# Kernel optimization log

Hardware: AMD Instinct MI355X
Metric: run time of the kernel (lower is better)

The kernel has to match this reference:

```python
import jax, jax.numpy as jnp
import numpy as np

B, S, D = 32, 512, 1024
H = 1024
Hh = H // 2
CYC = 3
EPS = 1e-6


def setup_inputs() -> dict:
    key = jax.random.key(0)
    ks = jax.random.split(key, 16)
    def rn(k, shape, scale):
        return (jax.random.normal(k, shape, dtype=jnp.float32) * scale)
    inp = {
        'x': rn(ks[0], (B, S, D), 1.0),
        'W_x': rn(ks[1], (D, H), 1.0 / np.sqrt(D)),
        'b_x': jnp.zeros((H,), jnp.float32),
        'W_h': rn(ks[2], (H, H), 1.0 / np.sqrt(H)),
        'b_h': jnp.zeros((H,), jnp.float32),
        'W_r': rn(ks[3], (D + H, H), 1.0 / np.sqrt(D + H)),
        'b_r': jnp.zeros((H,), jnp.float32),
        'W_s': rn(ks[4], (H, 3), 1.0 / np.sqrt(H)),
        'b_s': jnp.zeros((3,), jnp.float32),
        # Mobius coefficients (cycles, [re,im], Hh): a,d near identity, b,c small
        'mob_a': rn(ks[5], (CYC, 2, Hh), 0.01).at[:, 0, :].add(1.0),
        'mob_b': rn(ks[6], (CYC, 2, Hh), 0.01),
        'mob_c': rn(ks[7], (CYC, 2, Hh), 0.01),
        'mob_d': rn(ks[8], (CYC, 2, Hh), 0.01).at[:, 0, :].add(1.0),
        'W_o': rn(ks[9], (H, H), 1.0 / np.sqrt(H)),
        'b_o': jnp.zeros((H,), jnp.float32),
    }
    return inp


def _mobius(zo, zp, a, b, c, d):
    # elementwise complex Mobius transform z -> (a z + b) / (c z + d)
    a_re, a_im = a[0], a[1]
    b_re, b_im = b[0], b[1]
    c_re, c_im = c[0], c[1]
    d_re, d_im = d[0], d[1]
    num_re = a_re * zo - a_im * zp + b_re
    num_im = a_re * zp + a_im * zo + b_im
    den_re = c_re * zo - c_im * zp + d_re
    den_im = c_re * zp + c_im * zo + d_im
    den2 = den_re * den_re + den_im * den_im + EPS
    return ((num_re * den_re + num_im * den_im) / den2,
            (num_im * den_re - num_re * den_im) / den2)


def reference(x, W_x, b_x, W_h, b_h, W_r, b_r, W_s, b_s,
              mob_a, mob_b, mob_c, mob_d, W_o, b_o):
    Bx = x.shape[0]
    scales = jnp.array([1.0, 0.5, 0.25], dtype=x.dtype)

    def step(h, x_t):
        omega_h, pi_h = h                                  # (B, Hh) each
        h_cat = jnp.concatenate([omega_h, pi_h], axis=-1)  # (B, H)
        x_proj = jnp.tanh(x_t @ W_x + b_x)
        cand = jnp.tanh(x_proj + h_cat @ W_h + b_h)
        zo, zp = cand[:, :Hh], cand[:, Hh:]
        for k in range(CYC):
            zo, zp = _mobius(zo, zp, mob_a[k], mob_b[k], mob_c[k], mob_d[k])
        # adaptive evolution rate
        r = jax.nn.sigmoid(jnp.concatenate([x_t, h_cat], axis=-1) @ W_r + b_r)
        # multiscale evolution: softmax-mixed decay scale per batch element
        w = jax.nn.softmax(h_cat @ W_s + b_s, axis=-1)     # (B, 3)
        rate = r * (w @ scales)[:, None]                   # (B, H)
        ro, rp = rate[:, :Hh], rate[:, Hh:]
        new_o = (1.0 - ro) * omega_h + ro * zo
        new_p = (1.0 - rp) * pi_h + rp * zp
        out = jnp.tanh(jnp.concatenate([new_o, new_p], axis=-1) @ W_o + b_o)
        return (new_o, new_p), out

    h0 = (jnp.zeros((Bx, Hh), x.dtype), jnp.zeros((Bx, Hh), x.dtype))
    (of, pf), ys = jax.lax.scan(step, h0, jnp.swapaxes(x, 0, 1))
    output = jnp.swapaxes(ys, 0, 1)                        # (B, S, H)
    return output, of, pf
```

## Files before the change

### kernel.cpp

```cpp
#include <hip/hip_runtime.h>
#include <math.h>

typedef unsigned short u16;
typedef unsigned int u32;
typedef __attribute__((ext_vector_type(8))) short bf16x8;
typedef __attribute__((ext_vector_type(4))) float f32x4;

#define B_N 32
#define S_N 512
#define H_N 1024
#define HH_N 512
#define FRAME (B_N*H_N)
#define GBLK 32
#define EPS_F 1e-6f

#define MFMA16(a,b,c) __builtin_amdgcn_mfma_f32_16x16x32_bf16((a),(b),(c),0,0,0)
#define ATOM_ST(p,v) __hip_atomic_store((p),(v),__ATOMIC_RELAXED,__HIP_MEMORY_SCOPE_AGENT)

static __device__ __forceinline__ u16 f2bu(float v){
  union{float f; unsigned u;} x; x.f = v;
  unsigned r = x.u + 0x7FFFu + ((x.u>>16)&1u);
  return (u16)(r>>16);
}
static __device__ __forceinline__ float bu2f(u16 s){
  union{unsigned u; float f;} x; x.u = ((unsigned)s)<<16; return x.f;
}
static __device__ __forceinline__ bf16x8 ld8(const u16* p){
  return *reinterpret_cast<const bf16x8*>(p);
}
static __device__ __forceinline__ void cvt8(const float* p, bf16x8& hi, bf16x8& lo){
  #pragma unroll
  for(int j=0;j<8;j++){
    float v = p[j];
    u16 h = f2bu(v);
    hi[j] = (short)h;
    lo[j] = (short)f2bu(v - bu2f(h));
  }
}

__global__ __launch_bounds__(256) void k_trcvt(const float* __restrict__ src,
    u16* __restrict__ dh, u16* __restrict__ dl){
  __shared__ float tile[32][33];
  int c0 = blockIdx.x*32, k0 = blockIdx.y*32;
  int tx = threadIdx.x & 31, ty = threadIdx.x >> 5;
  for(int i=ty;i<32;i+=8) tile[i][tx] = src[(size_t)(k0+i)*H_N + c0 + tx];
  __syncthreads();
  for(int i=ty;i<32;i+=8){
    float v = tile[tx][i];
    u16 h = f2bu(v);
    dh[(size_t)(c0+i)*H_N + k0 + tx] = h;
    if(dl) dl[(size_t)(c0+i)*H_N + k0 + tx] = f2bu(v - bu2f(h));
  }
}

__global__ __launch_bounds__(256) void k_wspack(const float* __restrict__ Ws,
                                                u16* __restrict__ wsp){
  int gid = blockIdx.x*256 + threadIdx.x;
  int j = gid & 7, l = (gid>>3) & 63, ks = gid >> 9;
  int lr = l & 15, lg = l >> 4;
  int k = ks*32 + lg*8 + j;
  wsp[gid] = (lr < 3) ? f2bu(Ws[k*3 + lr]) : (u16)0;
}

__global__ __launch_bounds__(256) void k_pre(const float* __restrict__ x,
    const u16* __restrict__ WxTh, const u16* __restrict__ WxTl,
    const u16* __restrict__ WrxTh, const u16* __restrict__ WrxTl,
    const float* __restrict__ b_x,
    u16* __restrict__ xp, u16* __restrict__ xplo,
    u16* __restrict__ xr, u16* __restrict__ xrlo){
  int tid = threadIdx.x, l = tid&63, wid = tid>>6;
  int wm = wid>>1, wn = wid&1, lr = l&15, lg = l>>4;
  int mbase = blockIdx.y*64 + wm*32;
  int nblk = blockIdx.x*64;
  bool isX = (nblk < H_N);
  int nbase = nblk + wn*32;
  const u16* WTh = isX? WxTh : WrxTh;
  const u16* WTl = isX? WxTl : WrxTl;
  int nw0 = isX? nbase : (nbase - H_N);
  const float* ar[2]; const u16* brh[2]; const u16* brl[2];
  #pragma unroll
  for(int mt=0;mt<2;mt++){
    int m = mbase + mt*16 + lr;
    ar[mt] = x + ((size_t)(m & (B_N-1))*S_N + (m>>5))*H_N;
  }
  #pragma unroll
  for(int nt=0;nt<2;nt++){
    brh[nt] = WTh + (size_t)(nw0 + nt*16 + lr)*H_N;
    brl[nt] = WTl + (size_t)(nw0 + nt*16 + lr)*H_N;
  }
  f32x4 zz = {0.f,0.f,0.f,0.f};
  f32x4 acc[2][2] = {{zz,zz},{zz,zz}};
  for(int ks=0;ks<32;ks++){
    int ke = ks*32 + lg*8;
    bf16x8 ah[2], al[2], bh[2], bl[2];
    #pragma unroll
    for(int mt=0;mt<2;mt++) cvt8(ar[mt]+ke, ah[mt], al[mt]);
    #pragma unroll
    for(int nt=0;nt<2;nt++){ bh[nt] = ld8(brh[nt]+ke); bl[nt] = ld8(brl[nt]+ke); }
    #pragma unroll
    for(int mt=0;mt<2;mt++)
      #pragma unroll
      for(int nt=0;nt<2;nt++){
        acc[mt][nt] = MFMA16(ah[mt],bh[nt],acc[mt][nt]);
        acc[mt][nt] = MFMA16(al[mt],bh[nt],acc[mt][nt]);
        acc[mt][nt] = MFMA16(ah[mt],bl[nt],acc[mt][nt]);
      }
  }
  #pragma unroll
  for(int mt=0;mt<2;mt++)
    #pragma unroll
    for(int nt=0;nt<2;nt++){
      int n = nbase + nt*16 + lr;
      #pragma unroll
      for(int i=0;i<4;i++){
        int m = mbase + mt*16 + lg*4 + i;
        size_t idx = (size_t)m*H_N + (isX? n : (n - H_N));
        float v = acc[mt][nt][i];
        if(isX){
          float tv = tanhf(v + b_x[n]);
          u16 h = f2bu(tv);
          xp[idx] = h;
          if(xplo) xplo[idx] = f2bu(tv - bu2f(h));
        }else{
          u16 h = f2bu(v);
          xr[idx] = h;
          if(xrlo) xrlo[idx] = f2bu(v - bu2f(h));
        }
      }
    }
}

__global__ __launch_bounds__(256) void k_fin(const u16* __restrict__ hall,
    const u16* __restrict__ WoTh, const u16* __restrict__ WoTl,
    const float* __restrict__ b_o, float* __restrict__ out){
  int tid = threadIdx.x, l = tid&63, wid = tid>>6;
  int wm = wid>>1, wn = wid&1, lr = l&15, lg = l>>4;
  int mbase = blockIdx.y*64 + wm*32;
  int nbase = blockIdx.x*64 + wn*32;
  size_t arowB[2]; const u16* brh[2]; const u16* brl[2];
  #pragma unroll
  for(int mt=0;mt<2;mt++){
    int m = mbase + mt*16 + lr;
    arowB[mt] = (size_t)(m>>5)*FRAME + (size_t)(m&31)*32;
  }
  #pragma unroll
  for(int nt=0;nt<2;nt++){
    brh[nt] = WoTh + (size_t)(nbase + nt*16 + lr)*H_N;
    brl[nt] = WoTl + (size_t)(nbase + nt*16 + lr)*H_N;
  }
  int lgadd = (lg>>1)*1024 + (lg&1)*8;
  f32x4 zz = {0.f,0.f,0.f,0.f};
  f32x4 acc[2][2] = {{zz,zz},{zz,zz}};
  for(int ks=0;ks<32;ks++){
    int ke = ks*32 + lg*8;
    int abase = (2*(ks&15))*1024 + lgadd + ((ks>=16)?16:0);
    #pragma unroll
    for(int mt=0;mt<2;mt++){
      bf16x8 a = ld8(hall + arowB[mt] + abase);
      #pragma unroll
      for(int nt=0;nt<2;nt++){
        acc[mt][nt] = MFMA16(a, ld8(brh[nt]+ke), acc[mt][nt]);
        acc[mt][nt] = MFMA16(a, ld8(brl[nt]+ke), acc[mt][nt]);
      }
    }
  }
  #pragma unroll
  for(int mt=0;mt<2;mt++)
    #pragma unroll
    for(int nt=0;nt<2;nt++){
      int n = nbase + nt*16 + lr;
      float bo = b_o[n];
      #pragma unroll
      for(int i=0;i<4;i++){
        int m = mbase + mt*16 + lg*4 + i;
        int b = m & (B_N-1), t = m >> 5;
        out[((size_t)b*S_N + t)*H_N + n] = tanhf(acc[mt][nt][i] + bo);
      }
    }
}

__global__ __launch_bounds__(256) void k_recur(
    const u16* __restrict__ xp, const u16* __restrict__ xplo0,
    const u16* __restrict__ xr, const u16* __restrict__ xrlo0, int xlostep,
    const u16* __restrict__ WhTh, const u16* __restrict__ WhTl,
    const u16* __restrict__ WrTh, const u16* __restrict__ wsp,
    const float* __restrict__ b_h, const float* __restrict__ b_r,
    const float* __restrict__ b_s,
    const float* __restrict__ mob_a, const float* __restrict__ mob_b,
    const float* __restrict__ mob_c, const float* __restrict__ mob_d,
    const u16* __restrict__ zhi, u16* __restrict__ lob,
    u16* __restrict__ hall, float* __restrict__ hf, int* __restrict__ arr)
{
  __shared__ float Cred[32*84];
  __shared__ float Cs[32*84];
  __shared__ float mobp[16*25];
  __shared__ float bias[64];
  __shared__ float sbar[32];
  __shared__ float bsv[3];
  __shared__ float hfL[32][33];
  int tid = threadIdx.x, bid = blockIdx.x;
  int P0 = bid*16;
  int l = tid&63, kq = tid>>6;
  int lr = l&15, lg = l>>4;

  for(int idx=tid; idx<384; idx+=256){
    int j = idx/24, c = idx%24, cyc = c>>3, q = c&7;
    const float* arrp = (q<2)? mob_a : (q<4)? mob_b : (q<6)? mob_c : mob_d;
    mobp[j*25 + c] = arrp[cyc*H_N + (q&1)*HH_N + P0 + j];
  }
  if(tid < 64){
    int grp = tid>>4, jj = tid&15;
    bias[tid] = ((grp<2)? b_h : b_r)[P0 + jj + ((grp&1)? HH_N : 0)];
  } else if(tid < 67){
    bsv[tid-64] = b_s[tid-64];
  }
  for(int idx=tid; idx<32*33; idx+=256) (&hfL[0][0])[idx] = 0.f;

  const u16* bhOh = WhTh + (size_t)(P0 + lr)*H_N;
  const u16* bhOl = WhTl + (size_t)(P0 + lr)*H_N;
  const u16* bhPh = WhTh + (size_t)(P0 + HH_N + lr)*H_N;
  const u16* bhPl = WhTl + (size_t)(P0 + HH_N + lr)*H_N;
  const u16* brO  = WrTh + (size_t)(P0 + lr)*H_N;
  const u16* brP  = WrTh + (size_t)(P0 + HH_N + lr)*H_N;
  const u16* wps  = wsp + (size_t)(kq*8)*512 + l*8;
  int lgadd = (lg>>1)*1024 + (lg&1)*8 + ((kq>=2)?16:0);
  int row0t = lr*32, row1t = (16+lr)*32;
  int erow = tid>>3, ejj = (tid&7)*2;
  size_t ei0 = (size_t)erow*H_N + P0 + ejj;
  size_t ei1 = ei0 + HH_N;

  __syncthreads();

  for(int t=0; t<S_N; t++){
    const u16* hihB = (t==0)? zhi : (hall + (size_t)(t-1)*FRAME);
    const u16* hilB = lob + (size_t)(t&1)*FRAME;
    const u16* xp_t   = xp + (size_t)t*FRAME;
    const u16* xr_t   = xr + (size_t)t*FRAME;
    const u16* xplo_t = xplo0 + (size_t)t*xlostep;
    const u16* xrlo_t = xrlo0 + (size_t)t*xlostep;

    u32 pxpL = *(const u32*)(xp_t   + ei0);
    u32 pxpH = *(const u32*)(xp_t   + ei1);
    u32 ploL = *(const u32*)(xplo_t + ei0);
    u32 ploH = *(const u32*)(xplo_t + ei1);
    u32 pxrL = *(const u32*)(xr_t   + ei0);
    u32 pxrH = *(const u32*)(xr_t   + ei1);
    u32 prlL = *(const u32*)(xrlo_t + ei0);
    u32 prlH = *(const u32*)(xrlo_t + ei1);

    f32x4 zz = {0.f,0.f,0.f,0.f};
    f32x4 cO0=zz,cO1=zz,cP0=zz,cP1=zz,rOa=zz,rOb=zz,rPa=zz,rPb=zz,sA=zz,sB=zz;
    #pragma unroll
    for(int i=0;i<8;i++){
      int ke = (kq*8+i)*32 + lg*8;
      int abase = (2*((kq&1)*8+i))*1024 + lgadd;
      bf16x8 ah0 = ld8(hihB + abase + row0t);
      bf16x8 ah1 = ld8(hihB + abase + row1t);
      bf16x8 al0 = ld8(hilB + abase + row0t);
      bf16x8 al1 = ld8(hilB + abase + row1t);
      bf16x8 fOh = ld8(bhOh+ke), fOl = ld8(bhOl+ke);
      bf16x8 fPh = ld8(bhPh+ke), fPl = ld8(bhPl+ke);
      bf16x8 frO_ = ld8(brO+ke), frP_ = ld8(brP+ke);
      bf16x8 fs   = ld8(wps + i*512);
      cO0 = MFMA16(ah0,fOh,cO0); cO0 = MFMA16(al0,fOh,cO0); cO0 = MFMA16(ah0,fOl,cO0);
      cO1 = MFMA16(ah1,fOh,cO1); cO1 = MFMA16(al1,fOh,cO1); cO1 = MFMA16(ah1,fOl,cO1);
      cP0 = MFMA16(ah0,fPh,cP0); cP0 = MFMA16(al0,fPh,cP0); cP0 = MFMA16(ah0,fPl,cP0);
      cP1 = MFMA16(ah1,fPh,cP1); cP1 = MFMA16(al1,fPh,cP1); cP1 = MFMA16(ah1,fPl,cP1);
      rOa = MFMA16(ah0,frO_,rOa); rOa = MFMA16(al0,frO_,rOa);
      rOb = MFMA16(ah1,frO_,rOb); rOb = MFMA16(al1,frO_,rOb);
      rPa = MFMA16(ah0,frP_,rPa); rPa = MFMA16(al0,frP_,rPa);
      rPb = MFMA16(ah1,frP_,rPb); rPb = MFMA16(al1,frP_,rPb);
      sA  = MFMA16(ah0,fs, sA);  sA  = MFMA16(al0,fs, sA);
      sB  = MFMA16(ah1,fs, sB);  sB  = MFMA16(al1,fs, sB);
    }

    __syncthreads();
    float* D = (kq&1)? Cs : Cred;
    if(kq < 2){
      #pragma unroll
      for(int i=0;i<4;i++){
        int r0 = (lg*4+i)*84, r1 = (16+lg*4+i)*84;
        D[r0 +      lr] = cO0[i];  D[r1 +      lr] = cO1[i];
        D[r0 + 16 + lr] = cP0[i];  D[r1 + 16 + lr] = cP1[i];
        D[r0 + 32 + lr] = rOa[i];  D[r1 + 32 + lr] = rOb[i];
        D[r0 + 48 + lr] = rPa[i];  D[r1 + 48 + lr] = rPb[i];
        D[r0 + 64 + lr] = sA[i];   D[r1 + 64 + lr] = sB[i];
      }
    }
    __syncthreads();
    if(kq >= 2){
      #pragma unroll
      for(int i=0;i<4;i++){
        int r0 = (lg*4+i)*84, r1 = (16+lg*4+i)*84;
        D[r0 +      lr] += cO0[i];  D[r1 +      lr] += cO1[i];
        D[r0 + 16 + lr] += cP0[i];  D[r1 + 16 + lr] += cP1[i];
        D[r0 + 32 + lr] += rOa[i];  D[r1 + 32 + lr] += rOb[i];
        D[r0 + 48 + lr] += rPa[i];  D[r1 + 48 + lr] += rPb[i];
        D[r0 + 64 + lr] += sA[i];   D[r1 + 64 + lr] += sB[i];
      }
    }
    __syncthreads();
    for(int idx=tid; idx<2560; idx+=256){
      int r = idx/80, c = idx - r*80;
      Cred[r*84+c] += Cs[r*84+c];
    }
    __syncthreads();

    if(tid < 32){
      float l0 = Cred[tid*84+64] + bsv[0];
      float l1 = Cred[tid*84+65] + bsv[1];
      float l2 = Cred[tid*84+66] + bsv[2];
      float mx = fmaxf(l0, fmaxf(l1,l2));
      float e0 = expf(l0-mx), e1 = expf(l1-mx), e2 = expf(l2-mx);
      sbar[tid] = (e0 + 0.5f*e1 + 0.25f*e2) / (e0+e1+e2);
    }
    __syncthreads();

    {
      float sb = sbar[erow];
      u16 nob[2], npb[2], loO[2], loP[2];
      #pragma unroll
      for(int d=0; d<2; d++){
        int j = ejj + d;
        float xpv0 = bu2f((u16)(pxpL>>(16*d))) + bu2f((u16)(ploL>>(16*d)));
        float xpv1 = bu2f((u16)(pxpH>>(16*d))) + bu2f((u16)(ploH>>(16*d)));
        float xrv0 = bu2f((u16)(pxrL>>(16*d))) + bu2f((u16)(prlL>>(16*d)));
        float xrv1 = bu2f((u16)(pxrH>>(16*d))) + bu2f((u16)(prlH>>(16*d)));
        float zo = tanhf(xpv0 + Cred[erow*84 + j]      + bias[j]);
        float zp = tanhf(xpv1 + Cred[erow*84 + 16 + j] + bias[16+j]);
        float ro = 1.f/(1.f + expf(-(xrv0 + Cred[erow*84 + 32 + j] + bias[32+j])));
        float rp = 1.f/(1.f + expf(-(xrv1 + Cred[erow*84 + 48 + j] + bias[48+j])));
        const float* mp = &mobp[j*25];
        #pragma unroll
        for(int cy=0;cy<3;cy++){
          float are=mp[cy*8+0], aim=mp[cy*8+1], bre=mp[cy*8+2], bim=mp[cy*8+3];
          float cre=mp[cy*8+4], cim=mp[cy*8+5], dre=mp[cy*8+6], dim_=mp[cy*8+7];
          float nre = are*zo - aim*zp + bre;
          float nim = are*zp + aim*zo + bim;
          float de  = cre*zo - cim*zp + dre;
          float di  = cre*zp + cim*zo + dim_;
          float inv = 1.f/(de*de + di*di + EPS_F);
          float nzo = (nre*de + nim*di)*inv;
          float nzp = (nim*de - nre*di)*inv;
          zo = nzo; zp = nzp;
        }
        ro *= sb; rp *= sb;
        float ho = hfL[erow][j], hp2 = hfL[erow][16+j];
        float no  = (1.f-ro)*ho + ro*zo;
        float np2 = (1.f-rp)*hp2 + rp*zp;
        hfL[erow][j] = no; hfL[erow][16+j] = np2;
        nob[d] = f2bu(no);  npb[d] = f2bu(np2);
        loO[d] = f2bu(no  - bu2f(nob[d]));
        loP[d] = f2bu(np2 - bu2f(npb[d]));
      }
      size_t bb = (size_t)bid*1024 + (size_t)erow*32 + ejj;
      u16* hallT = hall + (size_t)t*FRAME;
      u16* lonT  = lob + (size_t)((t+1)&1)*FRAME;
      ATOM_ST((u32*)(hallT + bb),      (u32)nob[0] | ((u32)nob[1]<<16));
      ATOM_ST((u32*)(hallT + bb + 16), (u32)npb[0] | ((u32)npb[1]<<16));
      ATOM_ST((u32*)(lonT  + bb),      (u32)loO[0] | ((u32)loO[1]<<16));
      ATOM_ST((u32*)(lonT  + bb + 16), (u32)loP[0] | ((u32)loP[1]<<16));
    }

    __syncthreads();
    if(tid == 0)
      __hip_atomic_store(&arr[bid<<5], t+1, __ATOMIC_RELEASE, __HIP_MEMORY_SCOPE_AGENT);
    if(tid < GBLK){
      while(__hip_atomic_load(&arr[tid<<5], __ATOMIC_ACQUIRE, __HIP_MEMORY_SCOPE_AGENT) <= t)
        __builtin_amdgcn_s_sleep(1);
    }
    __syncthreads();
  }

  for(int idx=tid; idx<1024; idx+=256){
    int r = idx>>5, c = idx&31;
    int g = (c<16)? (P0+c) : (P0 + HH_N + (c-16));
    hf[(size_t)r*H_N + g] = hfL[r][c];
  }
}

__global__ __launch_bounds__(256) void k_tail(const float* __restrict__ hf,
                                              float* __restrict__ out){
  int i = blockIdx.x*256 + threadIdx.x;
  int b = i >> 10, c = i & 1023;
  float v = hf[(size_t)b*H_N + c];
  size_t base = (size_t)B_N*S_N*H_N;
  size_t idx = (c < HH_N) ? base + (size_t)b*HH_N + c
                          : base + (size_t)B_N*HH_N + (size_t)b*HH_N + (c - HH_N);
  out[idx] = v;
}

extern "C" void kernel_launch(void* const* d_in, const int* in_sizes, int n_in,
                              void* d_out, int out_size, void* d_ws, size_t ws_size,
                              hipStream_t stream)
{
  const float* x    = (const float*)d_in[0];
  const float* W_x  = (const float*)d_in[1];
  const float* b_x  = (const float*)d_in[2];
  const float* W_h  = (const float*)d_in[3];
  const float* b_h  = (const float*)d_in[4];
  const float* W_r  = (const float*)d_in[5];
  const float* b_r  = (const float*)d_in[6];
  const float* W_s  = (const float*)d_in[7];
  const float* b_s  = (const float*)d_in[8];
  const float* mob_a= (const float*)d_in[9];
  const float* mob_b= (const float*)d_in[10];
  const float* mob_c= (const float*)d_in[11];
  const float* mob_d= (const float*)d_in[12];
  const float* W_o  = (const float*)d_in[13];
  const float* b_o  = (const float*)d_in[14];
  float* out = (float*)d_out;

  char* ws = (char*)d_ws;
  size_t off = 0;
  auto carve = [&](size_t bytes)->char*{
    char* p = ws + off; off = (off + bytes + 255) & ~(size_t)255; return p;
  };
  int*   arr  = (int*)carve(4096);
  float* hf   = (float*)carve((size_t)FRAME*sizeof(float));
  u16*   zhi  = (u16*)carve((size_t)FRAME*sizeof(u16));
  u16*   lob  = (u16*)carve((size_t)2*FRAME*sizeof(u16));
  size_t hdr_bytes = off;
  u16*   WhTh = (u16*)carve((size_t)H_N*H_N*sizeof(u16));
  u16*   WhTl = (u16*)carve((size_t)H_N*H_N*sizeof(u16));
  u16*   WrTh = (u16*)carve((size_t)H_N*H_N*sizeof(u16));
  u16*   wsp  = (u16*)carve((size_t)32*512*sizeof(u16));
  u16*   hall = (u16*)carve((size_t)S_N*FRAME*sizeof(u16));
  u16*   xp   = (u16*)carve((size_t)S_N*FRAME*sizeof(u16));
  u16*   xr   = (u16*)carve((size_t)S_N*FRAME*sizeof(u16));
  size_t base_off = off;
  size_t lo_bytes = (size_t)S_N*FRAME*sizeof(u16);
  bool haslo = (ws_size >= base_off + 2*lo_bytes + 4096);
  u16* xplo = nullptr; u16* xrlo = nullptr;
  if(haslo){
    xplo = (u16*)carve(lo_bytes);
    xrlo = (u16*)carve(lo_bytes);
  }

  const size_t WSZ = (size_t)H_N*H_N;
  u16* WxTh  = hall;
  u16* WxTl  = hall + WSZ;
  u16* WrxTh = hall + 2*WSZ;
  u16* WrxTl = hall + 3*WSZ;
  u16* WoTh  = xp;
  u16* WoTl  = xp + WSZ;

  (void)hipMemsetAsync(d_ws, 0, hdr_bytes, stream);

  k_trcvt<<<dim3(32,32),256,0,stream>>>(W_h, WhTh, WhTl);
  k_trcvt<<<dim3(32,32),256,0,stream>>>(W_r + (size_t)H_N*H_N, WrTh, (u16*)nullptr);
  k_trcvt<<<dim3(32,32),256,0,stream>>>(W_x, WxTh, WxTl);
  k_trcvt<<<dim3(32,32),256,0,stream>>>(W_r, WrxTh, WrxTl);
  k_wspack<<<64,256,0,stream>>>(W_s, wsp);
  k_pre<<<dim3(32,256),256,0,stream>>>(x, WxTh, WxTl, WrxTh, WrxTl, b_x,
                                       xp, xplo, xr, xrlo);

  k_recur<<<GBLK,256,0,stream>>>(
      xp, haslo ? xplo : zhi, xr, haslo ? xrlo : zhi, haslo ? FRAME : 0,
      WhTh, WhTl, WrTh, wsp, b_h, b_r, b_s,
      mob_a, mob_b, mob_c, mob_d, zhi, lob, hall, hf, arr);

  k_trcvt<<<dim3(32,32),256,0,stream>>>(W_o, WoTh, WoTl);
  k_fin<<<dim3(16,256),256,0,stream>>>(hall, WoTh, WoTl, b_o, out);
  k_tail<<<128,256,0,stream>>>(hf, out);
}
```

Measured before the change: 5.687 ms.

## Replace grid barrier with per-producer flag polling and fuse partial-sum reduction

Removes the full grid-wide spin barrier at the end of each timestep. Instead, each wave polls the arrival flags of only the producer blocks whose hidden-state chunks it needs and runs the MFMA k-slices as soon as those chunks are ready. The four wave partial sums are now written to separate shared buffers and reduced in a single pass, and every thread computes the softmax scale itself, which removes several __syncthreads. The trade-offs are more polling traffic and data-dependent control flow inside the MFMA loop, and the memory ordering between the relaxed stores and the release flag becomes more delicate.

```diff
diff --git a/kernel.cpp b/kernel.cpp
--- a/kernel.cpp
+++ b/kernel.cpp
@@ -191,11 +191,9 @@
     const u16* __restrict__ zhi, u16* __restrict__ lob,
     u16* __restrict__ hall, float* __restrict__ hf, int* __restrict__ arr)
 {
-  __shared__ float Cred[32*84];
-  __shared__ float Cs[32*84];
+  __shared__ float Cpart[4][2688];
   __shared__ float mobp[16*25];
   __shared__ float bias[64];
-  __shared__ float sbar[32];
   __shared__ float bsv[3];
   __shared__ float hfL[32][33];
   int tid = threadIdx.x, bid = blockIdx.x;
@@ -225,6 +223,7 @@
   const u16* wps  = wsp + (size_t)(kq*8)*512 + l*8;
   int lgadd = (lg>>1)*1024 + (lg&1)*8 + ((kq>=2)?16:0);
   int row0t = lr*32, row1t = (16+lr)*32;
+  int ob = (kq&1)*16;
   int erow = tid>>3, ejj = (tid&7)*2;
   size_t ei0 = (size_t)erow*H_N + P0 + ejj;
   size_t ei1 = ei0 + HH_N;
@@ -250,74 +249,73 @@
 
     f32x4 zz = {0.f,0.f,0.f,0.f};
     f32x4 cO0=zz,cO1=zz,cP0=zz,cP1=zz,rOa=zz,rOb=zz,rPa=zz,rPb=zz,sA=zz,sB=zz;
-    #pragma unroll
-    for(int i=0;i<8;i++){
-      int ke = (kq*8+i)*32 + lg*8;
-      int abase = (2*((kq&1)*8+i))*1024 + lgadd;
-      bf16x8 ah0 = ld8(hihB + abase + row0t);
-      bf16x8 ah1 = ld8(hihB + abase + row1t);
-      bf16x8 al0 = ld8(hilB + abase + row0t);
-      bf16x8 al1 = ld8(hilB + abase + row1t);
-      bf16x8 fOh = ld8(bhOh+ke), fOl = ld8(bhOl+ke);
-      bf16x8 fPh = ld8(bhPh+ke), fPl = ld8(bhPl+ke);
-      bf16x8 frO_ = ld8(brO+ke), frP_ = ld8(brP+ke);
-      bf16x8 fs   = ld8(wps + i*512);
-      cO0 = MFMA16(ah0,fOh,cO0); cO0 = MFMA16(al0,fOh,cO0); cO0 = MFMA16(ah0,fOl,cO0);
-      cO1 = MFMA16(ah1,fOh,cO1); cO1 = MFMA16(al1,fOh,cO1); cO1 = MFMA16(ah1,fOl,cO1);
-      cP0 = MFMA16(ah0,fPh,cP0); cP0 = MFMA16(al0,fPh,cP0); cP0 = MFMA16(ah0,fPl,cP0);
-      cP1 = MFMA16(ah1,fPh,cP1); cP1 = MFMA16(al1,fPh,cP1); cP1 = MFMA16(ah1,fPl,cP1);
-      rOa = MFMA16(ah0,frO_,rOa); rOa = MFMA16(al0,frO_,rOa);
-      rOb = MFMA16(ah1,frO_,rOb); rOb = MFMA16(al1,frO_,rOb);
-      rPa = MFMA16(ah0,frP_,rPa); rPa = MFMA16(al0,frP_,rPa);
-      rPb = MFMA16(ah1,frP_,rPb); rPb = MFMA16(al1,frP_,rPb);
-      sA  = MFMA16(ah0,fs, sA);  sA  = MFMA16(al0,fs, sA);
-      sB  = MFMA16(ah1,fs, sB);  sB  = MFMA16(al1,fs, sB);
-    }
-
+
+    unsigned rem = 0xFFu;
+    while(rem){
+      int f = 0x7fffffff;
+      if(l < 16)
+        f = __hip_atomic_load(&arr[(ob + l)<<5], __ATOMIC_ACQUIRE, __HIP_MEMORY_SCOPE_AGENT);
+      unsigned long long bal = __ballot(f >= t);
+      unsigned own = (unsigned)bal & 0xFFFFu;
+      unsigned pr  = own & (own>>1) & 0x5555u;
+      while(pr){
+        int b2 = __ffs(pr)-1; pr &= pr-1;
+        int i = b2 >> 1;
+        if(!(rem & (1u<<i))) continue;
+        rem &= ~(1u<<i);
+        int ke = (kq*8+i)*32 + lg*8;
+        int abase = (2*((kq&1)*8+i))*1024 + lgadd;
+        bf16x8 ah0 = ld8(hihB + abase + row0t);
+        bf16x8 ah1 = ld8(hihB + abase + row1t);
+        bf16x8 al0 = ld8(hilB + abase + row0t);
+        bf16x8 al1 = ld8(hilB + abase + row1t);
+        bf16x8 fOh = ld8(bhOh+ke), fOl = ld8(bhOl+ke);
+        bf16x8 fPh = ld8(bhPh+ke), fPl = ld8(bhPl+ke);
+        bf16x8 frO_ = ld8(brO+ke), frP_ = ld8(brP+ke);
+        bf16x8 fs   = ld8(wps + i*512);
+        cO0 = MFMA16(ah0,fOh,cO0); cO0 = MFMA16(al0,fOh,cO0); cO0 = MFMA16(ah0,fOl,cO0);
+        cO1 = MFMA16(ah1,fOh,cO1); cO1 = MFMA16(al1,fOh,cO1); cO1 = MFMA16(ah1,fOl,cO1);
+        cP0 = MFMA16(ah0,fPh,cP0); cP0 = MFMA16(al0,fPh,cP0); cP0 = MFMA16(ah0,fPl,cP0);
+        cP1 = MFMA16(ah1,fPh,cP1); cP1 = MFMA16(al1,fPh,cP1); cP1 = MFMA16(ah1,fPl,cP1);
+        rOa = MFMA16(ah0,frO_,rOa); rOa = MFMA16(al0,frO_,rOa);
+        rOb = MFMA16(ah1,frO_,rOb); rOb = MFMA16(al1,frO_,rOb);
+        rPa = MFMA16(ah0,frP_,rPa); rPa = MFMA16(al0,frP_,rPa);
+        rPb = MFMA16(ah1,frP_,rPb); rPb = MFMA16(al1,frP_,rPb);
+        sA  = MFMA16(ah0,fs, sA);  sA  = MFMA16(al0,fs, sA);
+        sB  = MFMA16(ah1,fs, sB);  sB  = MFMA16(al1,fs, sB);
+      }
+      if(rem) __builtin_amdgcn_s_sleep(1);
+    }
+
+    float* W = Cpart[kq];
+    #pragma unroll
+    for(int i=0;i<4;i++){
+      int r0 = (lg*4+i)*84, r1 = (16+lg*4+i)*84;
+      W[r0 +      lr] = cO0[i];  W[r1 +      lr] = cO1[i];
+      W[r0 + 16 + lr] = cP0[i];  W[r1 + 16 + lr] = cP1[i];
+      W[r0 + 32 + lr] = rOa[i];  W[r1 + 32 + lr] = rOb[i];
+      W[r0 + 48 + lr] = rPa[i];  W[r1 + 48 + lr] = rPb[i];
+      W[r0 + 64 + lr] = sA[i];   W[r1 + 64 + lr] = sB[i];
+    }
     __syncthreads();
-    float* D = (kq&1)? Cs : Cred;
-    if(kq < 2){
-      #pragma unroll
-      for(int i=0;i<4;i++){
-        int r0 = (lg*4+i)*84, r1 = (16+lg*4+i)*84;
-        D[r0 +      lr] = cO0[i];  D[r1 +      lr] = cO1[i];
-        D[r0 + 16 + lr] = cP0[i];  D[r1 + 16 + lr] = cP1[i];
-        D[r0 + 32 + lr] = rOa[i];  D[r1 + 32 + lr] = rOb[i];
-        D[r0 + 48 + lr] = rPa[i];  D[r1 + 48 + lr] = rPb[i];
-        D[r0 + 64 + lr] = sA[i];   D[r1 + 64 + lr] = sB[i];
+    {
+      int r = tid>>3, c0m = (tid&7)*10;
+      #pragma unroll
+      for(int cc=0;cc<10;cc++){
+        int e = r*84 + c0m + cc;
+        Cpart[0][e] = Cpart[0][e] + Cpart[1][e] + Cpart[2][e] + Cpart[3][e];
       }
     }
     __syncthreads();
-    if(kq >= 2){
-      #pragma unroll
-      for(int i=0;i<4;i++){
-        int r0 = (lg*4+i)*84, r1 = (16+lg*4+i)*84;
-        D[r0 +      lr] += cO0[i];  D[r1 +      lr] += cO1[i];
-        D[r0 + 16 + lr] += cP0[i];  D[r1 + 16 + lr] += cP1[i];
-        D[r0 + 32 + lr] += rOa[i];  D[r1 + 32 + lr] += rOb[i];
-        D[r0 + 48 + lr] += rPa[i];  D[r1 + 48 + lr] += rPb[i];
-        D[r0 + 64 + lr] += sA[i];   D[r1 + 64 + lr] += sB[i];
-      }
-    }
-    __syncthreads();
-    for(int idx=tid; idx<2560; idx+=256){
-      int r = idx/80, c = idx - r*80;
-      Cred[r*84+c] += Cs[r*84+c];
-    }
-    __syncthreads();
-
-    if(tid < 32){
-      float l0 = Cred[tid*84+64] + bsv[0];
-      float l1 = Cred[tid*84+65] + bsv[1];
-      float l2 = Cred[tid*84+66] + bsv[2];
+
+    {
+      const float* C0 = Cpart[0];
+      float l0 = C0[erow*84+64] + bsv[0];
+      float l1 = C0[erow*84+65] + bsv[1];
+      float l2 = C0[erow*84+66] + bsv[2];
       float mx = fmaxf(l0, fmaxf(l1,l2));
       float e0 = expf(l0-mx), e1 = expf(l1-mx), e2 = expf(l2-mx);
-      sbar[tid] = (e0 + 0.5f*e1 + 0.25f*e2) / (e0+e1+e2);
-    }
-    __syncthreads();
-
-    {
-      float sb = sbar[erow];
+      float sb = (e0 + 0.5f*e1 + 0.25f*e2) / (e0+e1+e2);
       u16 nob[2], npb[2], loO[2], loP[2];
       #pragma unroll
       for(int d=0; d<2; d++){
@@ -326,10 +324,10 @@
         float xpv1 = bu2f((u16)(pxpH>>(16*d))) + bu2f((u16)(ploH>>(16*d)));
         float xrv0 = bu2f((u16)(pxrL>>(16*d))) + bu2f((u16)(prlL>>(16*d)));
         float xrv1 = bu2f((u16)(pxrH>>(16*d))) + bu2f((u16)(prlH>>(16*d)));
-        float zo = tanhf(xpv0 + Cred[erow*84 + j]      + bias[j]);
-        float zp = tanhf(xpv1 + Cred[erow*84 + 16 + j] + bias[16+j]);
-        float ro = 1.f/(1.f + expf(-(xrv0 + Cred[erow*84 + 32 + j] + bias[32+j])));
-        float rp = 1.f/(1.f + expf(-(xrv1 + Cred[erow*84 + 48 + j] + bias[48+j])));
+        float zo = tanhf(xpv0 + C0[erow*84 + j]      + bias[j]);
+        float zp = tanhf(xpv1 + C0[erow*84 + 16 + j] + bias[16+j]);
+        float ro = 1.f/(1.f + expf(-(xrv0 + C0[erow*84 + 32 + j] + bias[32+j])));
+        float rp = 1.f/(1.f + expf(-(xrv1 + C0[erow*84 + 48 + j] + bias[48+j])));
         const float* mp = &mobp[j*25];
         #pragma unroll
         for(int cy=0;cy<3;cy++){
@@ -365,11 +363,6 @@
     __syncthreads();
     if(tid == 0)
       __hip_atomic_store(&arr[bid<<5], t+1, __ATOMIC_RELEASE, __HIP_MEMORY_SCOPE_AGENT);
-    if(tid < GBLK){
-      while(__hip_atomic_load(&arr[tid<<5], __ATOMIC_ACQUIRE, __HIP_MEMORY_SCOPE_AGENT) <= t)
-        __builtin_amdgcn_s_sleep(1);
-    }
-    __syncthreads();
   }
 
   for(int idx=tid; idx<1024; idx+=256){
```

New measurement: 7.941 ms. +39.6%, slower.

## Relax grid-barrier polling, pack arrival flags, load shared hidden state via atomics

Applied to the files above, without the earlier changes.

Reworks the per-step cross-block barrier. Arrival flags are packed contiguously instead of padded to separate cache lines, and spinning uses relaxed loads with only an occasional acquire. Hidden-state fragment loads become relaxed agent-scope atomic loads, presumably so they read coherent data without acquire fences. The softmax scale is computed per thread, dropping one __syncthreads and the sbar buffer. Without a final acquire after the spin exits, memory ordering may be broken, and packing the flags risks contention on a shared cache line.

```diff
diff --git a/kernel.cpp b/kernel.cpp
--- a/kernel.cpp
+++ b/kernel.cpp
@@ -3,6 +3,7 @@
 
 typedef unsigned short u16;
 typedef unsigned int u32;
+typedef unsigned long long u64;
 typedef __attribute__((ext_vector_type(8))) short bf16x8;
 typedef __attribute__((ext_vector_type(4))) float f32x4;
 
@@ -27,6 +28,11 @@
 }
 static __device__ __forceinline__ bf16x8 ld8(const u16* p){
   return *reinterpret_cast<const bf16x8*>(p);
+}
+static __device__ __forceinline__ bf16x8 ldh16(const u16* p){
+  u64 a = __hip_atomic_load((const u64*)p,     __ATOMIC_RELAXED, __HIP_MEMORY_SCOPE_AGENT);
+  u64 b = __hip_atomic_load((const u64*)(p+4), __ATOMIC_RELAXED, __HIP_MEMORY_SCOPE_AGENT);
+  union{ u64 q[2]; bf16x8 v; } u; u.q[0]=a; u.q[1]=b; return u.v;
 }
 static __device__ __forceinline__ void cvt8(const float* p, bf16x8& hi, bf16x8& lo){
   #pragma unroll
@@ -191,11 +197,9 @@
     const u16* __restrict__ zhi, u16* __restrict__ lob,
     u16* __restrict__ hall, float* __restrict__ hf, int* __restrict__ arr)
 {
-  __shared__ float Cred[32*84];
-  __shared__ float Cs[32*84];
+  __shared__ float Cpart[4][2688];
   __shared__ float mobp[16*25];
   __shared__ float bias[64];
-  __shared__ float sbar[32];
   __shared__ float bsv[3];
   __shared__ float hfL[32][33];
   int tid = threadIdx.x, bid = blockIdx.x;
@@ -254,10 +258,10 @@
     for(int i=0;i<8;i++){
       int ke = (kq*8+i)*32 + lg*8;
       int abase = (2*((kq&1)*8+i))*1024 + lgadd;
-      bf16x8 ah0 = ld8(hihB + abase + row0t);
-      bf16x8 ah1 = ld8(hihB + abase + row1t);
-      bf16x8 al0 = ld8(hilB + abase + row0t);
-      bf16x8 al1 = ld8(hilB + abase + row1t);
+      bf16x8 ah0 = ldh16(hihB + abase + row0t);
+      bf16x8 ah1 = ldh16(hihB + abase + row1t);
+      bf16x8 al0 = ldh16(hilB + abase + row0t);
+      bf16x8 al1 = ldh16(hilB + abase + row1t);
       bf16x8 fOh = ld8(bhOh+ke), fOl = ld8(bhOl+ke);
       bf16x8 fPh = ld8(bhPh+ke), fPl = ld8(bhPl+ke);
       bf16x8 frO_ = ld8(brO+ke), frP_ = ld8(brP+ke);
@@ -275,7 +279,7 @@
     }
 
     __syncthreads();
-    float* D = (kq&1)? Cs : Cred;
+    float* D = Cpart[kq&1];
     if(kq < 2){
       #pragma unroll
       for(int i=0;i<4;i++){
@@ -302,22 +306,18 @@
     __syncthreads();
     for(int idx=tid; idx<2560; idx+=256){
       int r = idx/80, c = idx - r*80;
-      Cred[r*84+c] += Cs[r*84+c];
-    }
-    __syncthreads();
-
-    if(tid < 32){
-      float l0 = Cred[tid*84+64] + bsv[0];
-      float l1 = Cred[tid*84+65] + bsv[1];
-      float l2 = Cred[tid*84+66] + bsv[2];
+      Cpart[0][r*84+c] += Cpart[1][r*84+c];
+    }
+    __syncthreads();
+
+    {
+      const float* C0 = &Cpart[0][erow*84];
+      float l0 = C0[64] + bsv[0];
+      float l1 = C0[65] + bsv[1];
+      float l2 = C0[66] + bsv[2];
       float mx = fmaxf(l0, fmaxf(l1,l2));
       float e0 = expf(l0-mx), e1 = expf(l1-mx), e2 = expf(l2-mx);
-      sbar[tid] = (e0 + 0.5f*e1 + 0.25f*e2) / (e0+e1+e2);
-    }
-    __syncthreads();
-
-    {
-      float sb = sbar[erow];
+      float sb = (e0 + 0.5f*e1 + 0.25f*e2) / (e0+e1+e2);
       u16 nob[2], npb[2], loO[2], loP[2];
       #pragma unroll
       for(int d=0; d<2; d++){
@@ -326,10 +326,10 @@
         float xpv1 = bu2f((u16)(pxpH>>(16*d))) + bu2f((u16)(ploH>>(16*d)));
         float xrv0 = bu2f((u16)(pxrL>>(16*d))) + bu2f((u16)(prlL>>(16*d)));
         float xrv1 = bu2f((u16)(pxrH>>(16*d))) + bu2f((u16)(prlH>>(16*d)));
-        float zo = tanhf(xpv0 + Cred[erow*84 + j]      + bias[j]);
-        float zp = tanhf(xpv1 + Cred[erow*84 + 16 + j] + bias[16+j]);
-        float ro = 1.f/(1.f + expf(-(xrv0 + Cred[erow*84 + 32 + j] + bias[32+j])));
-        float rp = 1.f/(1.f + expf(-(xrv1 + Cred[erow*84 + 48 + j] + bias[48+j])));
+        float zo = tanhf(xpv0 + C0[j]      + bias[j]);
+        float zp = tanhf(xpv1 + C0[16 + j] + bias[16+j]);
+        float ro = 1.f/(1.f + expf(-(xrv0 + C0[32 + j] + bias[32+j])));
+        float rp = 1.f/(1.f + expf(-(xrv1 + C0[48 + j] + bias[48+j])));
         const float* mp = &mobp[j*25];
         #pragma unroll
         for(int cy=0;cy<3;cy++){
@@ -364,10 +364,16 @@
 
     __syncthreads();
     if(tid == 0)
-      __hip_atomic_store(&arr[bid<<5], t+1, __ATOMIC_RELEASE, __HIP_MEMORY_SCOPE_AGENT);
+      __hip_atomic_store(&arr[bid], t+1, __ATOMIC_RELEASE, __HIP_MEMORY_SCOPE_AGENT);
     if(tid < GBLK){
-      while(__hip_atomic_load(&arr[tid<<5], __ATOMIC_ACQUIRE, __HIP_MEMORY_SCOPE_AGENT) <= t)
+      int it = 0;
+      while(__hip_atomic_load(&arr[tid], __ATOMIC_RELAXED, __HIP_MEMORY_SCOPE_AGENT) <= t){
         __builtin_amdgcn_s_sleep(1);
+        if(++it >= 4096){
+          it = 0;
+          (void)__hip_atomic_load(&arr[tid], __ATOMIC_ACQUIRE, __HIP_MEMORY_SCOPE_AGENT);
+        }
+      }
     }
     __syncthreads();
   }
```

Result: slower. 6.409 ms (+12.7%).
